# Kernel optimization log

Measured on AMD Instinct MI355X. Metric: run time of the kernel, lower is better.

The kernel has to match this reference:

```python
import jax, jax.numpy as jnp
import numpy as np

B, H, W, C, HEADS, WS, SS = 32, 56, 56, 512, 16, 7, 3
HID = 4 * C
N = WS * WS          # tokens per window = 49
NW = (H // WS) * (W // WS)  # windows per image = 64
HD = C // HEADS
SCALE = HD ** -0.5

def _rel_index():
    coords = np.stack(np.meshgrid(np.arange(WS), np.arange(WS), indexing='ij'))
    cf = coords.reshape(2, -1)
    rel = (cf[:, :, None] - cf[:, None, :]).transpose(1, 2, 0)
    rel[..., 0] += WS - 1
    rel[..., 1] += WS - 1
    rel[..., 0] *= 2 * WS - 1
    return rel.sum(-1)  # [N, N]

REL_IDX = _rel_index()

def _attn_mask():
    # standard Swin SW-MSA mask: label 3x3 shifted regions, diff labels -> -100
    img = np.zeros((H, W), dtype=np.float32)
    cnt = 0
    for hs in (slice(0, -WS), slice(-WS, -SS), slice(-SS, None)):
        for ws_ in (slice(0, -WS), slice(-WS, -SS), slice(-SS, None)):
            img[hs, ws_] = cnt
            cnt += 1
    mw = img.reshape(H // WS, WS, W // WS, WS).transpose(0, 2, 1, 3).reshape(NW, N)
    diff = mw[:, None, :] - mw[:, :, None]
    return jnp.asarray(np.where(diff != 0, -100.0, 0.0).astype(np.float32))  # [NW, N, N]

ATTN_MASK = _attn_mask()

def layernorm(x, g, b, eps=1e-5):
    m = jnp.mean(x, -1, keepdims=True)
    v = jnp.mean((x - m) ** 2, -1, keepdims=True)
    return (x - m) * jax.lax.rsqrt(v + eps) * g + b

def setup_inputs():
    key = jax.random.key(0)
    ks = jax.random.split(key, 8)
    f32 = jnp.float32
    return {
        'x': jax.random.normal(ks[0], (B, H * W, C), f32),
        'norm1_g': jnp.ones((C,), f32), 'norm1_b': jnp.zeros((C,), f32),
        'qkv_w': jax.random.normal(ks[1], (3 * C, C), f32) * 0.02,
        'qkv_b': jnp.zeros((3 * C,), f32),
        'rel_bias': jax.random.normal(ks[2], ((2 * WS - 1) ** 2, HEADS), f32) * 0.02,
        'proj_w': jax.random.normal(ks[3], (C, C), f32) * 0.02,
        'proj_b': jnp.zeros((C,), f32),
        'norm2_g': jnp.ones((C,), f32), 'norm2_b': jnp.zeros((C,), f32),
        'mlp_w1': jax.random.normal(ks[4], (HID, C), f32) * 0.02,
        'mlp_b1': jnp.zeros((HID,), f32),
        'mlp_w2': jax.random.normal(ks[5], (C, HID), f32) * 0.02,
        'mlp_b2': jnp.zeros((C,), f32),
    }

def reference(x, norm1_g, norm1_b, qkv_w, qkv_b, rel_bias, proj_w, proj_b,
              norm2_g, norm2_b, mlp_w1, mlp_b1, mlp_w2, mlp_b2):
    skip = x
    h = layernorm(x, norm1_g, norm1_b).reshape(B, H, W, C)
    h = jnp.roll(h, (-SS, -SS), axis=(1, 2))  # cyclic shift
    # window partition -> [B*NW, N, C]
    h = h.reshape(B, H // WS, WS, W // WS, WS, C).transpose(0, 1, 3, 2, 4, 5).reshape(B * NW, N, C)
    qkv = (h @ qkv_w.T + qkv_b).reshape(B * NW, N, 3, HEADS, HD).transpose(2, 0, 3, 1, 4)
    q, k, v = qkv[0] * SCALE, qkv[1], qkv[2]  # [B*NW, HEADS, N, HD]
    attn = jnp.einsum('whnd,whmd->whnm', q, k)
    bias = rel_bias[REL_IDX.reshape(-1)].reshape(N, N, HEADS).transpose(2, 0, 1)
    attn = attn + bias[None]
    attn = attn.reshape(B, NW, HEADS, N, N) + ATTN_MASK[None, :, None]
    attn = jax.nn.softmax(attn, axis=-1).reshape(B * NW, HEADS, N, N)
    h = jnp.einsum('whnm,whmd->whnd', attn, v).transpose(0, 2, 1, 3).reshape(B * NW, N, C)
    h = h @ proj_w.T + proj_b
    # window reverse + reverse cyclic shift
    h = h.reshape(B, H // WS, W // WS, WS, WS, C).transpose(0, 1, 3, 2, 4, 5).reshape(B, H, W, C)
    h = jnp.roll(h, (SS, SS), axis=(1, 2)).reshape(B, H * W, C)
    x = skip + h
    m = layernorm(x, norm2_g, norm2_b)
    m = jax.nn.gelu(m @ mlp_w1.T + mlp_b1, approximate=False) @ mlp_w2.T + mlp_b2
    return x + m
```

## Files before the change

### kernel.cpp

```cpp
#include <hip/hip_runtime.h>
#include <cstdint>
#include <cstddef>

#define DI __device__ __forceinline__

typedef __bf16 bf16_t;
typedef __bf16 bf16x8 __attribute__((ext_vector_type(8)));
typedef float f32x4 __attribute__((ext_vector_type(4)));

static constexpr float SCALE = 0.17677669529663687f;

DI bf16_t f2b(float f) {
  uint32_t u = __builtin_bit_cast(uint32_t, f);
  u += 0x7fffu + ((u >> 16) & 1u);
  return __builtin_bit_cast(bf16_t, (uint16_t)(u >> 16));
}

DI void gld16(const void* g, void* l) {
  __builtin_amdgcn_global_load_lds(
      (const __attribute__((address_space(1))) uint32_t*)g,
      (__attribute__((address_space(3))) uint32_t*)l, 16, 0, 0);
}

__global__ __launch_bounds__(256)
void cvtw(const float* __restrict__ in, bf16_t* __restrict__ out, int n) {
  int i = (blockIdx.x * 256 + threadIdx.x) * 4;
  if (i >= n) return;
  float4 v = *(const float4*)(in + i);
  ushort4 o;
  o.x = __builtin_bit_cast(uint16_t, f2b(v.x));
  o.y = __builtin_bit_cast(uint16_t, f2b(v.y));
  o.z = __builtin_bit_cast(uint16_t, f2b(v.z));
  o.w = __builtin_bit_cast(uint16_t, f2b(v.w));
  *(ushort4*)(out + i) = o;
}

__global__ __launch_bounds__(256)
void bias_pre(const float* __restrict__ rel, float* __restrict__ bf) {
  int idx = blockIdx.x * 256 + threadIdx.x;
  int head = idx >> 12, t1 = (idx >> 6) & 63, t2 = idx & 63;
  float v = -1e30f;
  if (t1 < 49 && t2 < 49) {
    int i1 = t1 / 7, j1 = t1 - i1 * 7, i2 = t2 / 7, j2 = t2 - i2 * 7;
    v = rel[((i1 - i2 + 6) * 13 + (j1 - j2 + 6)) * 16 + head];
  }
  bf[idx] = v;
}

template<bool WIN>
__global__ __launch_bounds__(128)
void ln_kernel(const float* __restrict__ in, const float* __restrict__ g,
               const float* __restrict__ be, bf16_t* __restrict__ out)
{
  const int r = blockIdx.x;
  const int tid = threadIdx.x;
  long srow;
  if (WIN) {
    int bw = r / 49, t = r - bw * 49;
    int b = bw >> 6, w = bw & 63;
    int wh = w >> 3, ww = w & 7;
    int i = t / 7, j = t - i * 7;
    int hs = wh * 7 + i + 3; if (hs >= 56) hs -= 56;
    int wsr = ww * 7 + j + 3; if (wsr >= 56) wsr -= 56;
    srow = (long)b * 3136 + hs * 56 + wsr;
  } else {
    srow = r;
  }
  const float4 v = *(const float4*)(in + srow * 512 + tid * 4);
  float s = v.x + v.y + v.z + v.w;
  float sq = v.x * v.x + v.y * v.y + v.z * v.z + v.w * v.w;
#pragma unroll
  for (int m = 1; m < 64; m <<= 1) { s += __shfl_xor(s, m); sq += __shfl_xor(sq, m); }
  __shared__ float ls[2], lq[2];
  if ((tid & 63) == 0) { ls[tid >> 6] = s; lq[tid >> 6] = sq; }
  __syncthreads();
  s = ls[0] + ls[1]; sq = lq[0] + lq[1];
  const float mean = s * (1.f / 512.f);
  const float rs = rsqrtf(sq * (1.f / 512.f) - mean * mean + 1e-5f);
  const float4 gg = *(const float4*)(g + tid * 4);
  const float4 bb = *(const float4*)(be + tid * 4);
  ushort4 o;
  o.x = __builtin_bit_cast(uint16_t, f2b((v.x - mean) * rs * gg.x + bb.x));
  o.y = __builtin_bit_cast(uint16_t, f2b((v.y - mean) * rs * gg.y + bb.y));
  o.z = __builtin_bit_cast(uint16_t, f2b((v.z - mean) * rs * gg.z + bb.z));
  o.w = __builtin_bit_cast(uint16_t, f2b((v.w - mean) * rs * gg.w + bb.w));
  *(ushort4*)(out + (long)r * 512 + tid * 4) = o;
}

#define MFMA16(a, b, c) __builtin_amdgcn_mfma_f32_16x16x32_bf16((a), (b), (c), 0, 0, 0)

template<int EPI>
__global__ __launch_bounds__(1024, 4)
void gemm256(const bf16_t* __restrict__ A, const bf16_t* __restrict__ Bw,
             const float* __restrict__ bias, const float* __restrict__ extra,
             void* __restrict__ out0, void* __restrict__ out1v, void* __restrict__ out2v,
             const int K, const int NBN)
{
  __shared__ __align__(128) bf16_t lds[8][8192];
  const int tid = threadIdx.x, lane = tid & 63, wave = tid >> 6;
  const int NT = K >> 5;

  const int xcd = blockIdx.x & 7, j = blockIdx.x >> 3;
  const int G = 32 / NBN;
  if (j >= G * NBN) return;
  const int bmo = j / NBN;
  const int bn = j - bmo * NBN;
  const int m0 = xcd * 49;
  const int tiles = (49 - bmo + G - 1) / G;
  const int ST = tiles * NT;

  const int srow = tid >> 2, slot = tid & 3;
  const int chunk = slot ^ ((srow >> 1) & 3);
  const size_t strideA = (size_t)G * 256 * K;

  const bf16_t* pAs = A + ((size_t)(m0 + bmo) * 256 + srow) * K + chunk * 8;
  const bf16_t* pBs = Bw + ((size_t)bn * 256 + srow) * K + chunk * 8;
  int sS = 0, ktS = 0;

#define STG() do { \
    if (sS < ST) { \
      gld16(pAs + ktS * 32, &lds[ktS & 3][tid * 8]); \
      gld16(pBs + ktS * 32, &lds[4 + (ktS & 3)][tid * 8]); \
      ++sS; if (++ktS == NT) { ktS = 0; pAs += strideA; } \
    } \
  } while (0)

  const int fr = lane & 15, fkc = lane >> 4;
  const int wr = wave >> 2, wc = wave & 3;
  const int slotq = (fkc ^ ((fr >> 1) & 3)) << 3;
  const int aoff = (wr * 64 + fr) * 32 + slotq;
  const int boff = (wc * 64 + fr) * 32 + slotq;

  f32x4 acc[4][4] = {};

  STG(); STG(); STG();
  asm volatile("s_waitcnt vmcnt(4)");
  __builtin_amdgcn_s_barrier();
  __builtin_amdgcn_sched_barrier(0);

  int sG = 0;
  int bmC = m0 + bmo;
  const int rq = fkc * 4;
  float bs[4];
#pragma unroll
  for (int n = 0; n < 4; ++n) bs[n] = bias[bn * 256 + wc * 64 + n * 16 + fr];

  for (int t = 0; t < tiles; ++t) {
#pragma unroll 4
    for (int kt = 0; kt < NT; ++kt) {
      bf16x8 af[4], bq[4];
#pragma unroll
      for (int m = 0; m < 4; ++m) af[m] = *(const bf16x8*)&lds[kt & 3][aoff + m * 512];
#pragma unroll
      for (int n = 0; n < 4; ++n) bq[n] = *(const bf16x8*)&lds[4 + (kt & 3)][boff + n * 512];
      STG();
      __builtin_amdgcn_sched_barrier(0);
      __builtin_amdgcn_s_barrier();
      asm volatile("s_waitcnt lgkmcnt(0)");
      __builtin_amdgcn_sched_barrier(0);
      __builtin_amdgcn_s_setprio(1);
#pragma unroll
      for (int m = 0; m < 4; ++m)
#pragma unroll
        for (int n = 0; n < 4; ++n)
          acc[m][n] = MFMA16(af[m], bq[n], acc[m][n]);
      __builtin_amdgcn_s_setprio(0);
      __builtin_amdgcn_sched_barrier(0);
      if (sG + 3 < ST)      asm volatile("s_waitcnt vmcnt(4)");
      else if (sG + 2 < ST) asm volatile("s_waitcnt vmcnt(2)");
      else                  asm volatile("s_waitcnt vmcnt(0)");
      __builtin_amdgcn_s_barrier();
      __builtin_amdgcn_sched_barrier(0);
      ++sG;
    }
#pragma unroll
    for (int m = 0; m < 4; ++m) {
#pragma unroll
      for (int jj4 = 0; jj4 < 4; ++jj4) {
        const int grow = bmC * 256 + wr * 64 + m * 16 + rq + jj4;
        long obase = 0;
        if (EPI == 0) {
          int bwi = grow / 49, t_ = grow - bwi * 49;
          obase = ((long)bwi * 784 + t_) * 32;
        } else if (EPI == 1) {
          int bwi = grow / 49, t_ = grow - bwi * 49;
          int b = bwi >> 6, w = bwi & 63;
          int wh = w >> 3, ww = w & 7;
          int i = t_ / 7, jj = t_ - i * 7;
          int hs = wh * 7 + i + 3; if (hs >= 56) hs -= 56;
          int wsr = ww * 7 + jj + 3; if (wsr >= 56) wsr -= 56;
          obase = ((long)b * 3136 + hs * 56 + wsr) * 512;
        } else if (EPI == 2) {
          obase = (long)grow * 2048;
        } else {
          obase = (long)grow * 512;
        }
#pragma unroll
        for (int n = 0; n < 4; ++n) {
          const int gcol = bn * 256 + wc * 64 + n * 16 + fr;
          float v = acc[m][n][jj4] + bs[n];
          if (EPI == 0) {
            int part = gcol >> 9, head = (gcol >> 5) & 15, d = gcol & 31;
            if (part == 0) v *= SCALE;
            bf16_t* dst = (bf16_t*)(part == 0 ? out0 : (part == 1 ? out1v : out2v));
            dst[obase + (long)head * 1568 + d] = f2b(v);
          } else if (EPI == 1) {
            ((float*)out0)[obase + gcol] = v + extra[obase + gcol];
          } else if (EPI == 2) {
            float m2 = v * v;
            float z = v * fmaf(0.07135481627f, m2, 1.59576912161f);
            float e = __expf(z);
            float rr = __builtin_amdgcn_rcpf(e + 1.0f);
            ((bf16_t*)out0)[obase + gcol] = f2b(fmaf(-v, rr, v));
          } else {
            ((float*)out0)[obase + gcol] = v + extra[obase + gcol];
          }
        }
      }
    }
#pragma unroll
    for (int m = 0; m < 4; ++m)
#pragma unroll
      for (int n = 0; n < 4; ++n) acc[m][n] = (f32x4){0.f, 0.f, 0.f, 0.f};
    bmC += G;
  }
#undef STG
}

__global__ __launch_bounds__(256)
void attn_kernel(const bf16_t* __restrict__ qb, const bf16_t* __restrict__ kb,
                 const bf16_t* __restrict__ vb, const float* __restrict__ biasf,
                 bf16_t* __restrict__ aout)
{
  __shared__ bf16_t Q[64 * 32];
  __shared__ bf16_t Kl[64 * 32];
  __shared__ bf16_t Vt[32 * 64];
  __shared__ bf16_t Pl[4][16 * 64];
  const int bid = blockIdx.x;
  const int bw = bid >> 4, head = bid & 15;
  const int tid = threadIdx.x, lane = tid & 63, wave = tid >> 6;
  {
    uint4 z = {0u, 0u, 0u, 0u};
    *(uint4*)&Q[tid * 8] = z;
    *(uint4*)&Kl[tid * 8] = z;
    *(uint4*)&Vt[tid * 8] = z;
  }
  __syncthreads();
  const bf16_t* qsrc = qb + (long)bid * (49 * 32);
  const bf16_t* ksrc = kb + (long)bid * (49 * 32);
  const bf16_t* vsrc = vb + (long)bid * (49 * 32);
  if (tid < 196) {
    *(uint4*)&Q[tid * 8] = *(const uint4*)(qsrc + tid * 8);
    *(uint4*)&Kl[tid * 8] = *(const uint4*)(ksrc + tid * 8);
  }
  for (int e = tid; e < 1568; e += 256) {
    int t = e >> 5, d = e & 31;
    Vt[d * 64 + t] = vsrc[e];
  }
  __syncthreads();
  const int fr = lane & 15, fk = (lane >> 4) * 8, rq = (lane >> 4) * 4;
  bf16x8 aq = *(const bf16x8*)&Q[(wave * 16 + fr) * 32 + fk];
  f32x4 s[4];
#pragma unroll
  for (int n = 0; n < 4; ++n) {
    bf16x8 bk = *(const bf16x8*)&Kl[(n * 16 + fr) * 32 + fk];
    f32x4 z = {0.f, 0.f, 0.f, 0.f};
    s[n] = __builtin_amdgcn_mfma_f32_16x16x32_bf16(aq, bk, z, 0, 0, 0);
  }
  const int w = bw & 63;
  const bool wh7 = ((w >> 3) == 7), ww7 = ((w & 7) == 7);
  const float* bh = biasf + head * 4096;
#pragma unroll
  for (int j = 0; j < 4; ++j) {
    const int row = wave * 16 + rq + j;
    int i1 = row / 7, j1 = row - i1 * 7;
    bool b1h = wh7 && (i1 >= 4), b1w = ww7 && (j1 >= 4);
    float pv[4];
    float mx = -3.0e38f;
#pragma unroll
    for (int n = 0; n < 4; ++n) {
      const int col = n * 16 + fr;
      float v = s[n][j] + bh[row * 64 + col];
      if (wh7 || ww7) {
        int i2 = col / 7, j2 = col - i2 * 7;
        bool b2h = wh7 && (i2 >= 4), b2w = ww7 && (j2 >= 4);
        if ((b1h != b2h) || (b1w != b2w)) v -= 100.f;
      }
      pv[n] = v;
      mx = fmaxf(mx, v);
    }
#pragma unroll
    for (int msk = 1; msk < 16; msk <<= 1) mx = fmaxf(mx, __shfl_xor(mx, msk));
    float sm = 0.f;
#pragma unroll
    for (int n = 0; n < 4; ++n) { pv[n] = __expf(pv[n] - mx); sm += pv[n]; }
#pragma unroll
    for (int msk = 1; msk < 16; msk <<= 1) sm += __shfl_xor(sm, msk);
    const float inv = 1.f / sm;
#pragma unroll
    for (int n = 0; n < 4; ++n)
      Pl[wave][(rq + j) * 64 + n * 16 + fr] = f2b(pv[n] * inv);
  }
  __syncthreads();
  f32x4 o[2] = {};
#pragma unroll
  for (int kk = 0; kk < 2; ++kk) {
    bf16x8 pa = *(const bf16x8*)&Pl[wave][fr * 64 + kk * 32 + fk];
#pragma unroll
    for (int dt = 0; dt < 2; ++dt) {
      bf16x8 vv = *(const bf16x8*)&Vt[(dt * 16 + fr) * 64 + kk * 32 + fk];
      o[dt] = __builtin_amdgcn_mfma_f32_16x16x32_bf16(pa, vv, o[dt], 0, 0, 0);
    }
  }
#pragma unroll
  for (int j = 0; j < 4; ++j) {
    const int t1 = wave * 16 + rq + j;
    if (t1 < 49) {
      bf16_t* dst = aout + ((long)bw * 49 + t1) * 512 + head * 32;
      dst[fr] = f2b(o[0][j]);
      dst[16 + fr] = f2b(o[1][j]);
    }
  }
}

extern "C" void kernel_launch(void* const* d_in, const int* in_sizes, int n_in,
                              void* d_out, int out_size, void* d_ws, size_t ws_size,
                              hipStream_t stream)
{
  const float* x      = (const float*)d_in[0];
  const float* n1g    = (const float*)d_in[1];
  const float* n1b    = (const float*)d_in[2];
  const float* qkv_w  = (const float*)d_in[3];
  const float* qkv_b  = (const float*)d_in[4];
  const float* rel    = (const float*)d_in[5];
  const float* proj_w = (const float*)d_in[6];
  const float* proj_b = (const float*)d_in[7];
  const float* n2g    = (const float*)d_in[8];
  const float* n2b    = (const float*)d_in[9];
  const float* w1     = (const float*)d_in[10];
  const float* b1     = (const float*)d_in[11];
  const float* w2     = (const float*)d_in[12];
  const float* b2     = (const float*)d_in[13];

  char* ws = (char*)d_ws;
  bf16_t* Wqkv  = (bf16_t*)(ws + 0);
  bf16_t* Wproj = (bf16_t*)(ws + 1572864);
  bf16_t* Wm1   = (bf16_t*)(ws + 2097152);
  bf16_t* Wm2   = (bf16_t*)(ws + 4194304);
  float*  biasf = (float*)(ws + 6291456);
  const size_t ABYTES = (size_t)100352 * 512 * 2;
  const size_t P1 = 8388608;
  const size_t P2 = P1 + ABYTES + 1048576;
  bf16_t* xw      = (bf16_t*)(ws + P1);
  bf16_t* qbuf    = (bf16_t*)(ws + P2);
  bf16_t* kbuf    = (bf16_t*)(ws + P2 + ABYTES);
  bf16_t* vbuf    = (bf16_t*)(ws + P2 + 2 * ABYTES);
  bf16_t* attnout = xw;
  bf16_t* h2      = xw;
  bf16_t* hidden  = qbuf;

  cvtw<<<768, 256, 0, stream>>>(qkv_w, Wqkv, 1536 * 512);
  cvtw<<<256, 256, 0, stream>>>(proj_w, Wproj, 512 * 512);
  cvtw<<<1024, 256, 0, stream>>>(w1, Wm1, 2048 * 512);
  cvtw<<<1024, 256, 0, stream>>>(w2, Wm2, 512 * 2048);
  bias_pre<<<256, 256, 0, stream>>>(rel, biasf);

  ln_kernel<true><<<100352, 128, 0, stream>>>(x, n1g, n1b, xw);
  gemm256<0><<<256, 1024, 0, stream>>>(xw, Wqkv, qkv_b, nullptr,
                                       qbuf, kbuf, vbuf, 512, 6);
  attn_kernel<<<32768, 256, 0, stream>>>(qbuf, kbuf, vbuf, biasf, attnout);
  gemm256<1><<<256, 1024, 0, stream>>>(attnout, Wproj, proj_b, x,
                                       d_out, nullptr, nullptr, 512, 2);
  ln_kernel<false><<<100352, 128, 0, stream>>>((const float*)d_out, n2g, n2b, h2);
  gemm256<2><<<256, 1024, 0, stream>>>(h2, Wm1, b1, nullptr,
                                       hidden, nullptr, nullptr, 512, 8);
  gemm256<3><<<256, 1024, 0, stream>>>(hidden, Wm2, b2, (const float*)d_out,
                                       d_out, nullptr, nullptr, 2048, 2);
}
```

Baseline: 1.385 ms.

## Restructure GEMMs with resident B panel and register-staged A prefetch

Replaces the generic 256x256 gemm with two specialized kernels. The K=512 GEMMs (QKV, proj, MLP1) use 256x128 tiles, keep the whole B panel resident in LDS for the life of the block, and stream A through registers into a double-buffered LDS tile. The K=2048 MLP2 GEMM gets its own 512-thread kernel with register-staged A and B double buffering. Replacing the async global-to-LDS loads with register staging is meant to reduce per-k-step B reloads and synchronization, at the cost of more registers, lower MFMA density per wave and a changed tile walk order.

```diff
diff --git a/kernel.cpp b/kernel.cpp
--- a/kernel.cpp
+++ b/kernel.cpp
@@ -14,12 +14,6 @@
   uint32_t u = __builtin_bit_cast(uint32_t, f);
   u += 0x7fffu + ((u >> 16) & 1u);
   return __builtin_bit_cast(bf16_t, (uint16_t)(u >> 16));
-}
-
-DI void gld16(const void* g, void* l) {
-  __builtin_amdgcn_global_load_lds(
-      (const __attribute__((address_space(1))) uint32_t*)g,
-      (__attribute__((address_space(3))) uint32_t*)l, 16, 0, 0);
 }
 
 __global__ __launch_bounds__(256)
@@ -90,141 +84,281 @@
 #define MFMA16(a, b, c) __builtin_amdgcn_mfma_f32_16x16x32_bf16((a), (b), (c), 0, 0, 0)
 
 template<int EPI>
+DI void epi_store(int grow, int gcol, float v, const float* extra,
+                  void* out0, void* out1v, void* out2v)
+{
+  long obase = 0;
+  if (EPI == 0) {
+    int bwi = grow / 49, t_ = grow - bwi * 49;
+    obase = ((long)bwi * 784 + t_) * 32;
+  } else if (EPI == 1) {
+    int bwi = grow / 49, t_ = grow - bwi * 49;
+    int b = bwi >> 6, w = bwi & 63;
+    int wh = w >> 3, ww = w & 7;
+    int i = t_ / 7, jj = t_ - i * 7;
+    int hs = wh * 7 + i + 3; if (hs >= 56) hs -= 56;
+    int wsr = ww * 7 + jj + 3; if (wsr >= 56) wsr -= 56;
+    obase = ((long)b * 3136 + hs * 56 + wsr) * 512;
+  } else if (EPI == 2) {
+    obase = (long)grow * 2048;
+  } else {
+    obase = (long)grow * 512;
+  }
+  if (EPI == 0) {
+    int part = gcol >> 9, head = (gcol >> 5) & 15, d = gcol & 31;
+    if (part == 0) v *= SCALE;
+    bf16_t* dst = (bf16_t*)(part == 0 ? out0 : (part == 1 ? out1v : out2v));
+    dst[obase + (long)head * 1568 + d] = f2b(v);
+  } else if (EPI == 1) {
+    ((float*)out0)[obase + gcol] = v + extra[obase + gcol];
+  } else if (EPI == 2) {
+    float m2 = v * v;
+    float z = v * fmaf(0.07135481627f, m2, 1.59576912161f);
+    float e = __expf(z);
+    float rr = __builtin_amdgcn_rcpf(e + 1.0f);
+    ((bf16_t*)out0)[obase + gcol] = f2b(fmaf(-v, rr, v));
+  } else {
+    ((float*)out0)[obase + gcol] = v + extra[obase + gcol];
+  }
+}
+
+template<int EPI, int NBN>
 __global__ __launch_bounds__(1024, 4)
-void gemm256(const bf16_t* __restrict__ A, const bf16_t* __restrict__ Bw,
-             const float* __restrict__ bias, const float* __restrict__ extra,
-             void* __restrict__ out0, void* __restrict__ out1v, void* __restrict__ out2v,
-             const int K, const int NBN)
+void gemmR(const bf16_t* __restrict__ A, const bf16_t* __restrict__ Bw,
+           const float* __restrict__ bias, const float* __restrict__ extra,
+           void* __restrict__ out0, void* __restrict__ out1v, void* __restrict__ out2v)
 {
-  __shared__ __align__(128) bf16_t lds[8][8192];
+  constexpr int K = 512;
+  __shared__ __align__(128) bf16_t Alds[2][8192];
+  __shared__ __align__(128) bf16_t Blds[16][4096];
   const int tid = threadIdx.x, lane = tid & 63, wave = tid >> 6;
-  const int NT = K >> 5;
-
-  const int xcd = blockIdx.x & 7, j = blockIdx.x >> 3;
-  const int G = 32 / NBN;
-  if (j >= G * NBN) return;
-  const int bmo = j / NBN;
-  const int bn = j - bmo * NBN;
-  const int m0 = xcd * 49;
-  const int tiles = (49 - bmo + G - 1) / G;
-  const int ST = tiles * NT;
+  const int nWalk = 256 / NBN;
+  const int j = blockIdx.x;
+  if (j >= nWalk * NBN) return;
+  const int bn = j % NBN;
+  const int bm0 = j / NBN;
+  const int tiles = (392 - bm0 + nWalk - 1) / nWalk;
+
+  {
+    const int prow = tid >> 3, ps8 = tid & 7;
+    const bf16_t* bsrc = Bw + (size_t)(bn * 128 + prow) * K + ps8 * 4;
+    const int wslot = (((ps8 >> 1) ^ ((prow >> 1) & 3)) << 4) + (ps8 & 1) * 8;
+    uint2 tmp[16];
+#pragma unroll
+    for (int r = 0; r < 16; ++r) tmp[r] = *(const uint2*)(bsrc + r * 32);
+#pragma unroll
+    for (int r = 0; r < 16; ++r)
+      *(uint2*)((char*)&Blds[r][0] + prow * 64 + wslot) = tmp[r];
+  }
+  asm volatile("s_waitcnt vmcnt(0)");
 
   const int srow = tid >> 2, slot = tid & 3;
-  const int chunk = slot ^ ((srow >> 1) & 3);
-  const size_t strideA = (size_t)G * 256 * K;
-
-  const bf16_t* pAs = A + ((size_t)(m0 + bmo) * 256 + srow) * K + chunk * 8;
-  const bf16_t* pBs = Bw + ((size_t)bn * 256 + srow) * K + chunk * 8;
-  int sS = 0, ktS = 0;
-
-#define STG() do { \
-    if (sS < ST) { \
-      gld16(pAs + ktS * 32, &lds[ktS & 3][tid * 8]); \
-      gld16(pBs + ktS * 32, &lds[4 + (ktS & 3)][tid * 8]); \
-      ++sS; if (++ktS == NT) { ktS = 0; pAs += strideA; } \
-    } \
+  const int wby = srow * 64 + (((slot ^ ((srow >> 1) & 3))) << 4);
+  const bf16_t* pAs = A + (size_t)(bm0 * 256 + srow) * K + slot * 8;
+  int ktS = 0, bmS = bm0;
+  uint4 aq[8];
+
+#define ADV() do { \
+    if (++ktS == 16) { ktS = 0; bmS += nWalk; if (bmS < 392) pAs += (size_t)nWalk * 131072; } \
   } while (0)
+#define LOADQ(U) do { aq[U] = *(const uint4*)(pAs + ktS * 32); ADV(); } while (0)
 
   const int fr = lane & 15, fkc = lane >> 4;
-  const int wr = wave >> 2, wc = wave & 3;
+  const int wr = wave >> 1, wc = wave & 1;
+  const int slotq = (fkc ^ ((fr >> 1) & 3)) << 3;
+  const int aoff = (wr * 32 + fr) * 32 + slotq;
+  const int boff = (wc * 64 + fr) * 32 + slotq;
+
+  f32x4 acc[2][4] = {};
+
+  LOADQ(0); LOADQ(1); LOADQ(2); LOADQ(3); LOADQ(4); LOADQ(5); LOADQ(6); LOADQ(7);
+  asm volatile("s_waitcnt vmcnt(7)");
+  __builtin_amdgcn_sched_barrier(0);
+  *(uint4*)((char*)&Alds[0][0] + wby) = aq[0];
+  asm volatile("s_waitcnt lgkmcnt(0)");
+  __builtin_amdgcn_s_barrier();
+  __builtin_amdgcn_sched_barrier(0);
+
+  const int rq = fkc * 4;
+  float bs[4];
+#pragma unroll
+  for (int n = 0; n < 4; ++n) bs[n] = bias[bn * 128 + wc * 64 + n * 16 + fr];
+
+  for (int t = 0; t < tiles; ++t) {
+#pragma unroll
+    for (int kt = 0; kt < 16; ++kt) {
+      const int u = kt & 7;
+      bf16x8 af0 = *(const bf16x8*)&Alds[kt & 1][aoff];
+      bf16x8 af1 = *(const bf16x8*)&Alds[kt & 1][aoff + 512];
+      bf16x8 b0 = *(const bf16x8*)&Blds[kt][boff];
+      bf16x8 b1 = *(const bf16x8*)&Blds[kt][boff + 512];
+      bf16x8 b2 = *(const bf16x8*)&Blds[kt][boff + 1024];
+      bf16x8 b3 = *(const bf16x8*)&Blds[kt][boff + 1536];
+      LOADQ(u);
+      asm volatile("s_waitcnt lgkmcnt(0)");
+      __builtin_amdgcn_sched_barrier(0);
+      __builtin_amdgcn_s_setprio(1);
+      acc[0][0] = MFMA16(af0, b0, acc[0][0]);
+      acc[0][1] = MFMA16(af0, b1, acc[0][1]);
+      acc[0][2] = MFMA16(af0, b2, acc[0][2]);
+      acc[0][3] = MFMA16(af0, b3, acc[0][3]);
+      acc[1][0] = MFMA16(af1, b0, acc[1][0]);
+      acc[1][1] = MFMA16(af1, b1, acc[1][1]);
+      acc[1][2] = MFMA16(af1, b2, acc[1][2]);
+      acc[1][3] = MFMA16(af1, b3, acc[1][3]);
+      __builtin_amdgcn_s_setprio(0);
+      __builtin_amdgcn_sched_barrier(0);
+      asm volatile("s_waitcnt vmcnt(7)");
+      __builtin_amdgcn_sched_barrier(0);
+      *(uint4*)((char*)&Alds[(kt + 1) & 1][0] + wby) = aq[(u + 1) & 7];
+      asm volatile("s_waitcnt lgkmcnt(0)");
+      __builtin_amdgcn_s_barrier();
+      __builtin_amdgcn_sched_barrier(0);
+    }
+    const int bmC = bm0 + t * nWalk;
+#pragma unroll
+    for (int m = 0; m < 2; ++m)
+#pragma unroll
+      for (int jj = 0; jj < 4; ++jj) {
+        const int grow = bmC * 256 + wr * 32 + m * 16 + rq + jj;
+#pragma unroll
+        for (int n = 0; n < 4; ++n) {
+          const int gcol = bn * 128 + wc * 64 + n * 16 + fr;
+          epi_store<EPI>(grow, gcol, acc[m][n][jj] + bs[n], extra, out0, out1v, out2v);
+        }
+      }
+#pragma unroll
+    for (int m = 0; m < 2; ++m)
+#pragma unroll
+      for (int n = 0; n < 4; ++n) acc[m][n] = (f32x4){0.f, 0.f, 0.f, 0.f};
+  }
+#undef LOADQ
+#undef ADV
+}
+
+__global__ __launch_bounds__(512, 2)
+void gemmS(const bf16_t* __restrict__ A, const bf16_t* __restrict__ Bw,
+           const float* __restrict__ bias, const float* __restrict__ extra,
+           void* __restrict__ out0)
+{
+  constexpr int K = 2048, NBN = 4, nWalk = 64;
+  __shared__ __align__(128) bf16_t Alds[2][8192];
+  __shared__ __align__(128) bf16_t Blds2[2][4096];
+  const int tid = threadIdx.x, lane = tid & 63, wave = tid >> 6;
+  const int j = blockIdx.x;
+  const int bn = j % NBN;
+  const int bm0 = j / NBN;
+  const int tiles = (392 - bm0 + nWalk - 1) / nWalk;
+
+  const int srow2 = tid >> 1, s0 = (tid & 1) * 2;
+  const int brow = tid >> 2, bslot = tid & 3;
+  const bf16_t* pA0 = A + (size_t)(bm0 * 256 + srow2) * K + s0 * 8;
+  const bf16_t* pB0 = Bw + (size_t)(bn * 128 + brow) * K + bslot * 8;
+  const int wbyA0 = srow2 * 64 + ((s0 ^ ((srow2 >> 1) & 3)) << 4);
+  const int wbyA1 = srow2 * 64 + (((s0 + 1) ^ ((srow2 >> 1) & 3)) << 4);
+  const int wbyB = brow * 64 + ((bslot ^ ((brow >> 1) & 3)) << 4);
+  int ktS = 0, bmS = bm0;
+  uint4 aqA0[8], aqA1[8], aqB[8];
+
+#define ADVS() do { \
+    if (++ktS == 64) { ktS = 0; bmS += nWalk; if (bmS < 392) pA0 += (size_t)nWalk * 524288; } \
+  } while (0)
+#define LOADQS(U) do { \
+    aqA0[U] = *(const uint4*)(pA0 + ktS * 32); \
+    aqA1[U] = *(const uint4*)(pA0 + ktS * 32 + 8); \
+    aqB[U]  = *(const uint4*)(pB0 + ktS * 32); \
+    ADVS(); \
+  } while (0)
+
+  const int fr = lane & 15, fkc = lane >> 4;
+  const int wr = wave >> 1, wc = wave & 1;
   const int slotq = (fkc ^ ((fr >> 1) & 3)) << 3;
   const int aoff = (wr * 64 + fr) * 32 + slotq;
   const int boff = (wc * 64 + fr) * 32 + slotq;
 
   f32x4 acc[4][4] = {};
 
-  STG(); STG(); STG();
-  asm volatile("s_waitcnt vmcnt(4)");
+  LOADQS(0); LOADQS(1); LOADQS(2); LOADQS(3);
+  LOADQS(4); LOADQS(5); LOADQS(6); LOADQS(7);
+  asm volatile("s_waitcnt vmcnt(21)");
+  __builtin_amdgcn_sched_barrier(0);
+  *(uint4*)((char*)&Alds[0][0] + wbyA0) = aqA0[0];
+  *(uint4*)((char*)&Alds[0][0] + wbyA1) = aqA1[0];
+  *(uint4*)((char*)&Blds2[0][0] + wbyB) = aqB[0];
+  asm volatile("s_waitcnt lgkmcnt(0)");
   __builtin_amdgcn_s_barrier();
   __builtin_amdgcn_sched_barrier(0);
 
-  int sG = 0;
-  int bmC = m0 + bmo;
   const int rq = fkc * 4;
   float bs[4];
 #pragma unroll
-  for (int n = 0; n < 4; ++n) bs[n] = bias[bn * 256 + wc * 64 + n * 16 + fr];
+  for (int n = 0; n < 4; ++n) bs[n] = bias[bn * 128 + wc * 64 + n * 16 + fr];
 
   for (int t = 0; t < tiles; ++t) {
-#pragma unroll 4
-    for (int kt = 0; kt < NT; ++kt) {
-      bf16x8 af[4], bq[4];
-#pragma unroll
-      for (int m = 0; m < 4; ++m) af[m] = *(const bf16x8*)&lds[kt & 3][aoff + m * 512];
-#pragma unroll
-      for (int n = 0; n < 4; ++n) bq[n] = *(const bf16x8*)&lds[4 + (kt & 3)][boff + n * 512];
-      STG();
-      __builtin_amdgcn_sched_barrier(0);
-      __builtin_amdgcn_s_barrier();
-      asm volatile("s_waitcnt lgkmcnt(0)");
-      __builtin_amdgcn_sched_barrier(0);
-      __builtin_amdgcn_s_setprio(1);
-#pragma unroll
-      for (int m = 0; m < 4; ++m)
-#pragma unroll
-        for (int n = 0; n < 4; ++n)
-          acc[m][n] = MFMA16(af[m], bq[n], acc[m][n]);
-      __builtin_amdgcn_s_setprio(0);
-      __builtin_amdgcn_sched_barrier(0);
-      if (sG + 3 < ST)      asm volatile("s_waitcnt vmcnt(4)");
-      else if (sG + 2 < ST) asm volatile("s_waitcnt vmcnt(2)");
-      else                  asm volatile("s_waitcnt vmcnt(0)");
-      __builtin_amdgcn_s_barrier();
-      __builtin_amdgcn_sched_barrier(0);
-      ++sG;
+#pragma unroll 1
+    for (int g = 0; g < 8; ++g) {
+#pragma unroll
+      for (int u = 0; u < 8; ++u) {
+        const int par = u & 1;
+        bf16x8 af0 = *(const bf16x8*)&Alds[par][aoff];
+        bf16x8 af1 = *(const bf16x8*)&Alds[par][aoff + 512];
+        bf16x8 af2 = *(const bf16x8*)&Alds[par][aoff + 1024];
+        bf16x8 af3 = *(const bf16x8*)&Alds[par][aoff + 1536];
+        bf16x8 b0 = *(const bf16x8*)&Blds2[par][boff];
+        bf16x8 b1 = *(const bf16x8*)&Blds2[par][boff + 512];
+        bf16x8 b2 = *(const bf16x8*)&Blds2[par][boff + 1024];
+        bf16x8 b3 = *(const bf16x8*)&Blds2[par][boff + 1536];
+        LOADQS(u);
+        asm volatile("s_waitcnt lgkmcnt(0)");
+        __builtin_amdgcn_sched_barrier(0);
+        __builtin_amdgcn_s_setprio(1);
+        acc[0][0] = MFMA16(af0, b0, acc[0][0]);
+        acc[0][1] = MFMA16(af0, b1, acc[0][1]);
+        acc[0][2] = MFMA16(af0, b2, acc[0][2]);
+        acc[0][3] = MFMA16(af0, b3, acc[0][3]);
+        acc[1][0] = MFMA16(af1, b0, acc[1][0]);
+        acc[1][1] = MFMA16(af1, b1, acc[1][1]);
+        acc[1][2] = MFMA16(af1, b2, acc[1][2]);
+        acc[1][3] = MFMA16(af1, b3, acc[1][3]);
+        acc[2][0] = MFMA16(af2, b0, acc[2][0]);
+        acc[2][1] = MFMA16(af2, b1, acc[2][1]);
+        acc[2][2] = MFMA16(af2, b2, acc[2][2]);
+        acc[2][3] = MFMA16(af2, b3, acc[2][3]);
+        acc[3][0] = MFMA16(af3, b0, acc[3][0]);
+        acc[3][1] = MFMA16(af3, b1, acc[3][1]);
+        acc[3][2] = MFMA16(af3, b2, acc[3][2]);
+        acc[3][3] = MFMA16(af3, b3, acc[3][3]);
+        __builtin_amdgcn_s_setprio(0);
+        __builtin_amdgcn_sched_barrier(0);
+        asm volatile("s_waitcnt vmcnt(21)");
+        __builtin_amdgcn_sched_barrier(0);
+        *(uint4*)((char*)&Alds[par ^ 1][0] + wbyA0) = aqA0[(u + 1) & 7];
+        *(uint4*)((char*)&Alds[par ^ 1][0] + wbyA1) = aqA1[(u + 1) & 7];
+        *(uint4*)((char*)&Blds2[par ^ 1][0] + wbyB) = aqB[(u + 1) & 7];
+        asm volatile("s_waitcnt lgkmcnt(0)");
+        __builtin_amdgcn_s_barrier();
+        __builtin_amdgcn_sched_barrier(0);
+      }
     }
-#pragma unroll
-    for (int m = 0; m < 4; ++m) {
-#pragma unroll
-      for (int jj4 = 0; jj4 < 4; ++jj4) {
-        const int grow = bmC * 256 + wr * 64 + m * 16 + rq + jj4;
-        long obase = 0;
-        if (EPI == 0) {
-          int bwi = grow / 49, t_ = grow - bwi * 49;
-          obase = ((long)bwi * 784 + t_) * 32;
-        } else if (EPI == 1) {
-          int bwi = grow / 49, t_ = grow - bwi * 49;
-          int b = bwi >> 6, w = bwi & 63;
-          int wh = w >> 3, ww = w & 7;
-          int i = t_ / 7, jj = t_ - i * 7;
-          int hs = wh * 7 + i + 3; if (hs >= 56) hs -= 56;
-          int wsr = ww * 7 + jj + 3; if (wsr >= 56) wsr -= 56;
-          obase = ((long)b * 3136 + hs * 56 + wsr) * 512;
-        } else if (EPI == 2) {
-          obase = (long)grow * 2048;
-        } else {
-          obase = (long)grow * 512;
-        }
+    const int bmC = bm0 + t * nWalk;
+#pragma unroll
+    for (int m = 0; m < 4; ++m)
+#pragma unroll
+      for (int jj = 0; jj < 4; ++jj) {
+        const int grow = bmC * 256 + wr * 64 + m * 16 + rq + jj;
 #pragma unroll
         for (int n = 0; n < 4; ++n) {
-          const int gcol = bn * 256 + wc * 64 + n * 16 + fr;
-          float v = acc[m][n][jj4] + bs[n];
-          if (EPI == 0) {
-            int part = gcol >> 9, head = (gcol >> 5) & 15, d = gcol & 31;
-            if (part == 0) v *= SCALE;
-            bf16_t* dst = (bf16_t*)(part == 0 ? out0 : (part == 1 ? out1v : out2v));
-            dst[obase + (long)head * 1568 + d] = f2b(v);
-          } else if (EPI == 1) {
-            ((float*)out0)[obase + gcol] = v + extra[obase + gcol];
-          } else if (EPI == 2) {
-            float m2 = v * v;
-            float z = v * fmaf(0.07135481627f, m2, 1.59576912161f);
-            float e = __expf(z);
-            float rr = __builtin_amdgcn_rcpf(e + 1.0f);
-            ((bf16_t*)out0)[obase + gcol] = f2b(fmaf(-v, rr, v));
-          } else {
-            ((float*)out0)[obase + gcol] = v + extra[obase + gcol];
-          }
+          const int gcol = bn * 128 + wc * 64 + n * 16 + fr;
+          epi_store<3>(grow, gcol, acc[m][n][jj] + bs[n], extra, out0, nullptr, nullptr);
         }
       }
-    }
 #pragma unroll
     for (int m = 0; m < 4; ++m)
 #pragma unroll
       for (int n = 0; n < 4; ++n) acc[m][n] = (f32x4){0.f, 0.f, 0.f, 0.f};
-    bmC += G;
-  }
-#undef STG
+  }
+#undef LOADQS
+#undef ADVS
 }
 
 __global__ __launch_bounds__(256)
@@ -366,14 +500,10 @@
   bias_pre<<<256, 256, 0, stream>>>(rel, biasf);
 
   ln_kernel<true><<<100352, 128, 0, stream>>>(x, n1g, n1b, xw);
-  gemm256<0><<<256, 1024, 0, stream>>>(xw, Wqkv, qkv_b, nullptr,
-                                       qbuf, kbuf, vbuf, 512, 6);
+  gemmR<0, 12><<<256, 1024, 0, stream>>>(xw, Wqkv, qkv_b, nullptr, qbuf, kbuf, vbuf);
   attn_kernel<<<32768, 256, 0, stream>>>(qbuf, kbuf, vbuf, biasf, attnout);
-  gemm256<1><<<256, 1024, 0, stream>>>(attnout, Wproj, proj_b, x,
-                                       d_out, nullptr, nullptr, 512, 2);
+  gemmR<1, 4><<<256, 1024, 0, stream>>>(attnout, Wproj, proj_b, x, d_out, nullptr, nullptr);
   ln_kernel<false><<<100352, 128, 0, stream>>>((const float*)d_out, n2g, n2b, h2);
-  gemm256<2><<<256, 1024, 0, stream>>>(h2, Wm1, b1, nullptr,
-                                       hidden, nullptr, nullptr, 512, 8);
-  gemm256<3><<<256, 1024, 0, stream>>>(hidden, Wm2, b2, (const float*)d_out,
-                                       d_out, nullptr, nullptr, 2048, 2);
-}
+  gemmR<2, 16><<<256, 1024, 0, stream>>>(h2, Wm1, b1, nullptr, hidden, nullptr, nullptr);
+  gemmS<<<256, 512, 0, stream>>>(hidden, Wm2, b2, (const float*)d_out, d_out);
+}
```

Measured after the change: 3.792 ms. 174% more time.

## Halve GEMM block to 8 waves with 128x64 per-wave tiles

Applied to the files above, without the earlier changes.

The 256x256 GEMM tile now runs on 512 threads (8 waves) instead of 1024. Each wave computes a 128x64 sub-tile with 8x4 MFMA accumulators, and each thread issues four LDS-direct global loads per stage instead of two. This raises operand reuse per wave and reduces per-block LDS read traffic and barrier participants. In exchange it doubles accumulator registers per thread, which limits occupancy, and gives fewer waves to hide latency. The epilogue is moved into a helper function with unchanged semantics.

```diff
diff --git a/kernel.cpp b/kernel.cpp
--- a/kernel.cpp
+++ b/kernel.cpp
@@ -90,13 +90,52 @@
 #define MFMA16(a, b, c) __builtin_amdgcn_mfma_f32_16x16x32_bf16((a), (b), (c), 0, 0, 0)
 
 template<int EPI>
-__global__ __launch_bounds__(1024, 4)
+DI void epi_store(int grow, int gcol, float v, const float* extra,
+                  void* out0, void* out1v, void* out2v)
+{
+  long obase = 0;
+  if (EPI == 0) {
+    int bwi = grow / 49, t_ = grow - bwi * 49;
+    obase = ((long)bwi * 784 + t_) * 32;
+  } else if (EPI == 1) {
+    int bwi = grow / 49, t_ = grow - bwi * 49;
+    int b = bwi >> 6, w = bwi & 63;
+    int wh = w >> 3, ww = w & 7;
+    int i = t_ / 7, jj = t_ - i * 7;
+    int hs = wh * 7 + i + 3; if (hs >= 56) hs -= 56;
+    int wsr = ww * 7 + jj + 3; if (wsr >= 56) wsr -= 56;
+    obase = ((long)b * 3136 + hs * 56 + wsr) * 512;
+  } else if (EPI == 2) {
+    obase = (long)grow * 2048;
+  } else {
+    obase = (long)grow * 512;
+  }
+  if (EPI == 0) {
+    int part = gcol >> 9, head = (gcol >> 5) & 15, d = gcol & 31;
+    if (part == 0) v *= SCALE;
+    bf16_t* dst = (bf16_t*)(part == 0 ? out0 : (part == 1 ? out1v : out2v));
+    dst[obase + (long)head * 1568 + d] = f2b(v);
+  } else if (EPI == 1) {
+    ((float*)out0)[obase + gcol] = v + extra[obase + gcol];
+  } else if (EPI == 2) {
+    float m2 = v * v;
+    float z = v * fmaf(0.07135481627f, m2, 1.59576912161f);
+    float e = __expf(z);
+    float rr = __builtin_amdgcn_rcpf(e + 1.0f);
+    ((bf16_t*)out0)[obase + gcol] = f2b(fmaf(-v, rr, v));
+  } else {
+    ((float*)out0)[obase + gcol] = v + extra[obase + gcol];
+  }
+}
+
+template<int EPI>
+__global__ __launch_bounds__(512, 2)
 void gemm256(const bf16_t* __restrict__ A, const bf16_t* __restrict__ Bw,
              const float* __restrict__ bias, const float* __restrict__ extra,
              void* __restrict__ out0, void* __restrict__ out1v, void* __restrict__ out2v,
              const int K, const int NBN)
 {
-  __shared__ __align__(128) bf16_t lds[8][8192];
+  __shared__ __align__(128) bf16_t lds[4][2][8192];
   const int tid = threadIdx.x, lane = tid & 63, wave = tid >> 6;
   const int NT = K >> 5;
 
@@ -111,6 +150,7 @@
 
   const int srow = tid >> 2, slot = tid & 3;
   const int chunk = slot ^ ((srow >> 1) & 3);
+  const size_t rowK = (size_t)128 * K;
   const size_t strideA = (size_t)G * 256 * K;
 
   const bf16_t* pAs = A + ((size_t)(m0 + bmo) * 256 + srow) * K + chunk * 8;
@@ -119,8 +159,13 @@
 
 #define STG() do { \
     if (sS < ST) { \
-      gld16(pAs + ktS * 32, &lds[ktS & 3][tid * 8]); \
-      gld16(pBs + ktS * 32, &lds[4 + (ktS & 3)][tid * 8]); \
+      const int _b = sS & 3; \
+      const bf16_t* _pa = pAs + ktS * 32; \
+      const bf16_t* _pb = pBs + ktS * 32; \
+      gld16(_pa, &lds[_b][0][tid * 8]); \
+      gld16(_pa + rowK, &lds[_b][0][tid * 8 + 4096]); \
+      gld16(_pb, &lds[_b][1][tid * 8]); \
+      gld16(_pb + rowK, &lds[_b][1][tid * 8 + 4096]); \
       ++sS; if (++ktS == NT) { ktS = 0; pAs += strideA; } \
     } \
   } while (0)
@@ -128,31 +173,32 @@
   const int fr = lane & 15, fkc = lane >> 4;
   const int wr = wave >> 2, wc = wave & 3;
   const int slotq = (fkc ^ ((fr >> 1) & 3)) << 3;
-  const int aoff = (wr * 64 + fr) * 32 + slotq;
+  const int aoff = (wr * 128 + fr) * 32 + slotq;
   const int boff = (wc * 64 + fr) * 32 + slotq;
 
-  f32x4 acc[4][4] = {};
+  f32x4 acc[8][4] = {};
 
   STG(); STG(); STG();
-  asm volatile("s_waitcnt vmcnt(4)");
+  asm volatile("s_waitcnt vmcnt(8)");
   __builtin_amdgcn_s_barrier();
   __builtin_amdgcn_sched_barrier(0);
 
   int sG = 0;
-  int bmC = m0 + bmo;
   const int rq = fkc * 4;
   float bs[4];
 #pragma unroll
   for (int n = 0; n < 4; ++n) bs[n] = bias[bn * 256 + wc * 64 + n * 16 + fr];
 
   for (int t = 0; t < tiles; ++t) {
+    const int bmC = m0 + bmo + t * G;
 #pragma unroll 4
     for (int kt = 0; kt < NT; ++kt) {
-      bf16x8 af[4], bq[4];
-#pragma unroll
-      for (int m = 0; m < 4; ++m) af[m] = *(const bf16x8*)&lds[kt & 3][aoff + m * 512];
-#pragma unroll
-      for (int n = 0; n < 4; ++n) bq[n] = *(const bf16x8*)&lds[4 + (kt & 3)][boff + n * 512];
+      const int b = kt & 3;
+      bf16x8 af[8], bq[4];
+#pragma unroll
+      for (int m = 0; m < 8; ++m) af[m] = *(const bf16x8*)&lds[b][0][aoff + m * 512];
+#pragma unroll
+      for (int n = 0; n < 4; ++n) bq[n] = *(const bf16x8*)&lds[b][1][boff + n * 512];
       STG();
       __builtin_amdgcn_sched_barrier(0);
       __builtin_amdgcn_s_barrier();
@@ -160,69 +206,34 @@
       __builtin_amdgcn_sched_barrier(0);
       __builtin_amdgcn_s_setprio(1);
 #pragma unroll
-      for (int m = 0; m < 4; ++m)
+      for (int m = 0; m < 8; ++m)
 #pragma unroll
         for (int n = 0; n < 4; ++n)
           acc[m][n] = MFMA16(af[m], bq[n], acc[m][n]);
       __builtin_amdgcn_s_setprio(0);
       __builtin_amdgcn_sched_barrier(0);
-      if (sG + 3 < ST)      asm volatile("s_waitcnt vmcnt(4)");
-      else if (sG + 2 < ST) asm volatile("s_waitcnt vmcnt(2)");
-      else                  asm volatile("s_waitcnt vmcnt(0)");
+      if (sG + 4 <= ST)      asm volatile("s_waitcnt vmcnt(8)");
+      else if (sG + 3 == ST) asm volatile("s_waitcnt vmcnt(4)");
+      else                   asm volatile("s_waitcnt vmcnt(0)");
       __builtin_amdgcn_s_barrier();
       __builtin_amdgcn_sched_barrier(0);
       ++sG;
     }
 #pragma unroll
-    for (int m = 0; m < 4; ++m) {
-#pragma unroll
-      for (int jj4 = 0; jj4 < 4; ++jj4) {
-        const int grow = bmC * 256 + wr * 64 + m * 16 + rq + jj4;
-        long obase = 0;
-        if (EPI == 0) {
-          int bwi = grow / 49, t_ = grow - bwi * 49;
-          obase = ((long)bwi * 784 + t_) * 32;
-        } else if (EPI == 1) {
-          int bwi = grow / 49, t_ = grow - bwi * 49;
-          int b = bwi >> 6, w = bwi & 63;
-          int wh = w >> 3, ww = w & 7;
-          int i = t_ / 7, jj = t_ - i * 7;
-          int hs = wh * 7 + i + 3; if (hs >= 56) hs -= 56;
-          int wsr = ww * 7 + jj + 3; if (wsr >= 56) wsr -= 56;
-          obase = ((long)b * 3136 + hs * 56 + wsr) * 512;
-        } else if (EPI == 2) {
-          obase = (long)grow * 2048;
-        } else {
-          obase = (long)grow * 512;
-        }
+    for (int m = 0; m < 8; ++m)
+#pragma unroll
+      for (int jj = 0; jj < 4; ++jj) {
+        const int grow = bmC * 256 + wr * 128 + m * 16 + rq + jj;
 #pragma unroll
         for (int n = 0; n < 4; ++n) {
           const int gcol = bn * 256 + wc * 64 + n * 16 + fr;
-          float v = acc[m][n][jj4] + bs[n];
-          if (EPI == 0) {
-            int part = gcol >> 9, head = (gcol >> 5) & 15, d = gcol & 31;
-            if (part == 0) v *= SCALE;
-            bf16_t* dst = (bf16_t*)(part == 0 ? out0 : (part == 1 ? out1v : out2v));
-            dst[obase + (long)head * 1568 + d] = f2b(v);
-          } else if (EPI == 1) {
-            ((float*)out0)[obase + gcol] = v + extra[obase + gcol];
-          } else if (EPI == 2) {
-            float m2 = v * v;
-            float z = v * fmaf(0.07135481627f, m2, 1.59576912161f);
-            float e = __expf(z);
-            float rr = __builtin_amdgcn_rcpf(e + 1.0f);
-            ((bf16_t*)out0)[obase + gcol] = f2b(fmaf(-v, rr, v));
-          } else {
-            ((float*)out0)[obase + gcol] = v + extra[obase + gcol];
-          }
+          epi_store<EPI>(grow, gcol, acc[m][n][jj] + bs[n], extra, out0, out1v, out2v);
         }
       }
-    }
-#pragma unroll
-    for (int m = 0; m < 4; ++m)
+#pragma unroll
+    for (int m = 0; m < 8; ++m)
 #pragma unroll
       for (int n = 0; n < 4; ++n) acc[m][n] = (f32x4){0.f, 0.f, 0.f, 0.f};
-    bmC += G;
   }
 #undef STG
 }
@@ -366,14 +377,14 @@
   bias_pre<<<256, 256, 0, stream>>>(rel, biasf);
 
   ln_kernel<true><<<100352, 128, 0, stream>>>(x, n1g, n1b, xw);
-  gemm256<0><<<256, 1024, 0, stream>>>(xw, Wqkv, qkv_b, nullptr,
-                                       qbuf, kbuf, vbuf, 512, 6);
+  gemm256<0><<<256, 512, 0, stream>>>(xw, Wqkv, qkv_b, nullptr,
+                                      qbuf, kbuf, vbuf, 512, 6);
   attn_kernel<<<32768, 256, 0, stream>>>(qbuf, kbuf, vbuf, biasf, attnout);
-  gemm256<1><<<256, 1024, 0, stream>>>(attnout, Wproj, proj_b, x,
-                                       d_out, nullptr, nullptr, 512, 2);
+  gemm256<1><<<256, 512, 0, stream>>>(attnout, Wproj, proj_b, x,
+                                      d_out, nullptr, nullptr, 512, 2);
   ln_kernel<false><<<100352, 128, 0, stream>>>((const float*)d_out, n2g, n2b, h2);
-  gemm256<2><<<256, 1024, 0, stream>>>(h2, Wm1, b1, nullptr,
-                                       hidden, nullptr, nullptr, 512, 8);
-  gemm256<3><<<256, 1024, 0, stream>>>(hidden, Wm2, b2, (const float*)d_out,
-                                       d_out, nullptr, nullptr, 2048, 2);
-}
+  gemm256<2><<<256, 512, 0, stream>>>(h2, Wm1, b1, nullptr,
+                                      hidden, nullptr, nullptr, 512, 8);
+  gemm256<3><<<256, 512, 0, stream>>>(hidden, Wm2, b2, (const float*)d_out,
+                                      d_out, nullptr, nullptr, 2048, 2);
+}
```

Result: no change. 1.377 ms (-0.6%).

## Replace direct-to-LDS GEMM with register-staged double-buffered 256x128 tiles

Applied to the files above, without the earlier changes.

The 256x256, 1024-thread GEMM that used global_load_lds with a 4-stage LDS ring is replaced by a 512-thread kernel using 256x128 tiles. Global loads now go into registers three k-steps ahead and are written into a two-slot LDS double buffer, with one barrier per k-step. Tiles are distributed across blocks as a flat (m,n) tile index strided by 32, and the epilogue moves into a helper function. The aim is better occupancy and balance, at the cost of more register pressure and extra LDS write instructions.

```diff
diff --git a/kernel.cpp b/kernel.cpp
--- a/kernel.cpp
+++ b/kernel.cpp
@@ -14,12 +14,6 @@
   uint32_t u = __builtin_bit_cast(uint32_t, f);
   u += 0x7fffu + ((u >> 16) & 1u);
   return __builtin_bit_cast(bf16_t, (uint16_t)(u >> 16));
-}
-
-DI void gld16(const void* g, void* l) {
-  __builtin_amdgcn_global_load_lds(
-      (const __attribute__((address_space(1))) uint32_t*)g,
-      (__attribute__((address_space(3))) uint32_t*)l, 16, 0, 0);
 }
 
 __global__ __launch_bounds__(256)
@@ -90,72 +84,121 @@
 #define MFMA16(a, b, c) __builtin_amdgcn_mfma_f32_16x16x32_bf16((a), (b), (c), 0, 0, 0)
 
 template<int EPI>
-__global__ __launch_bounds__(1024, 4)
-void gemm256(const bf16_t* __restrict__ A, const bf16_t* __restrict__ Bw,
-             const float* __restrict__ bias, const float* __restrict__ extra,
-             void* __restrict__ out0, void* __restrict__ out1v, void* __restrict__ out2v,
-             const int K, const int NBN)
-{
-  __shared__ __align__(128) bf16_t lds[8][8192];
+DI void epi_store(int grow, int gcol, float v, const float* extra,
+                  void* out0, void* out1v, void* out2v)
+{
+  long obase = 0;
+  if (EPI == 0) {
+    int bwi = grow / 49, t_ = grow - bwi * 49;
+    obase = ((long)bwi * 784 + t_) * 32;
+  } else if (EPI == 1) {
+    int bwi = grow / 49, t_ = grow - bwi * 49;
+    int b = bwi >> 6, w = bwi & 63;
+    int wh = w >> 3, ww = w & 7;
+    int i = t_ / 7, jj = t_ - i * 7;
+    int hs = wh * 7 + i + 3; if (hs >= 56) hs -= 56;
+    int wsr = ww * 7 + jj + 3; if (wsr >= 56) wsr -= 56;
+    obase = ((long)b * 3136 + hs * 56 + wsr) * 512;
+  } else if (EPI == 2) {
+    obase = (long)grow * 2048;
+  } else {
+    obase = (long)grow * 512;
+  }
+  if (EPI == 0) {
+    int part = gcol >> 9, head = (gcol >> 5) & 15, d = gcol & 31;
+    if (part == 0) v *= SCALE;
+    bf16_t* dst = (bf16_t*)(part == 0 ? out0 : (part == 1 ? out1v : out2v));
+    dst[obase + (long)head * 1568 + d] = f2b(v);
+  } else if (EPI == 1) {
+    ((float*)out0)[obase + gcol] = v + extra[obase + gcol];
+  } else if (EPI == 2) {
+    float m2 = v * v;
+    float z = v * fmaf(0.07135481627f, m2, 1.59576912161f);
+    float e = __expf(z);
+    float rr = __builtin_amdgcn_rcpf(e + 1.0f);
+    ((bf16_t*)out0)[obase + gcol] = f2b(fmaf(-v, rr, v));
+  } else {
+    ((float*)out0)[obase + gcol] = v + extra[obase + gcol];
+  }
+}
+
+template<int EPI, int NBN>
+__global__ __launch_bounds__(512, 2)
+void gemmP(const bf16_t* __restrict__ A, const bf16_t* __restrict__ Bw,
+           const float* __restrict__ bias, const float* __restrict__ extra,
+           void* __restrict__ out0, void* __restrict__ out1v, void* __restrict__ out2v,
+           const int K)
+{
+  __shared__ __align__(128) bf16_t ldsA[2][8192];
+  __shared__ __align__(128) bf16_t ldsB[2][4096];
   const int tid = threadIdx.x, lane = tid & 63, wave = tid >> 6;
   const int NT = K >> 5;
-
   const int xcd = blockIdx.x & 7, j = blockIdx.x >> 3;
-  const int G = 32 / NBN;
-  if (j >= G * NBN) return;
-  const int bmo = j / NBN;
-  const int bn = j - bmo * NBN;
   const int m0 = xcd * 49;
-  const int tiles = (49 - bmo + G - 1) / G;
-  const int ST = tiles * NT;
-
-  const int srow = tid >> 2, slot = tid & 3;
-  const int chunk = slot ^ ((srow >> 1) & 3);
-  const size_t strideA = (size_t)G * 256 * K;
-
-  const bf16_t* pAs = A + ((size_t)(m0 + bmo) * 256 + srow) * K + chunk * 8;
-  const bf16_t* pBs = Bw + ((size_t)bn * 256 + srow) * K + chunk * 8;
-  int sS = 0, ktS = 0;
-
-#define STG() do { \
-    if (sS < ST) { \
-      gld16(pAs + ktS * 32, &lds[ktS & 3][tid * 8]); \
-      gld16(pBs + ktS * 32, &lds[4 + (ktS & 3)][tid * 8]); \
-      ++sS; if (++ktS == NT) { ktS = 0; pAs += strideA; } \
+  const int ntileX = 49 * NBN;
+  const int tiles = (ntileX - j + 31) >> 5;
+
+  const int arow = tid >> 1, ac = (tid & 1) * 2;
+  const int brow = tid >> 2, bc = tid & 3;
+  const int awb0 = arow * 64 + ((ac ^ ((arow >> 1) & 3)) << 4);
+  const int awb1 = arow * 64 + (((ac + 1) ^ ((arow >> 1) & 3)) << 4);
+  const int bwb  = brow * 64 + ((bc ^ ((brow >> 1) & 3)) << 4);
+
+  int ktS = 0, tS = j;
+  const bf16_t* pA = A + ((size_t)(m0 + tS / NBN) * 256 + arow) * K + ac * 8;
+  const bf16_t* pB = Bw + ((size_t)(tS % NBN) * 128 + brow) * K + bc * 8;
+  uint4 qA0[4], qA1[4], qB[4];
+
+#define ISSUE(SLOT) do { \
+    qA0[SLOT] = *(const uint4*)(pA + ktS * 32); \
+    qA1[SLOT] = *(const uint4*)(pA + ktS * 32 + 8); \
+    qB[SLOT]  = *(const uint4*)(pB + ktS * 32); \
+    if (++ktS == NT) { \
+      ktS = 0; tS += 32; \
+      if (tS < ntileX) { \
+        pA = A + ((size_t)(m0 + tS / NBN) * 256 + arow) * K + ac * 8; \
+        pB = Bw + ((size_t)(tS % NBN) * 128 + brow) * K + bc * 8; \
+      } \
     } \
   } while (0)
 
+#define COMMIT(SLOT, BUF) do { \
+    *(uint4*)((char*)&ldsA[BUF][0] + awb0) = qA0[SLOT]; \
+    *(uint4*)((char*)&ldsA[BUF][0] + awb1) = qA1[SLOT]; \
+    *(uint4*)((char*)&ldsB[BUF][0] + bwb)  = qB[SLOT]; \
+  } while (0)
+
   const int fr = lane & 15, fkc = lane >> 4;
-  const int wr = wave >> 2, wc = wave & 3;
+  const int wr = wave >> 1, wc = wave & 1;
   const int slotq = (fkc ^ ((fr >> 1) & 3)) << 3;
   const int aoff = (wr * 64 + fr) * 32 + slotq;
   const int boff = (wc * 64 + fr) * 32 + slotq;
 
   f32x4 acc[4][4] = {};
 
-  STG(); STG(); STG();
-  asm volatile("s_waitcnt vmcnt(4)");
+  ISSUE(0); ISSUE(1); ISSUE(2);
+  COMMIT(0, 0);
+  asm volatile("s_waitcnt lgkmcnt(0)");
   __builtin_amdgcn_s_barrier();
   __builtin_amdgcn_sched_barrier(0);
 
-  int sG = 0;
-  int bmC = m0 + bmo;
   const int rq = fkc * 4;
-  float bs[4];
-#pragma unroll
-  for (int n = 0; n < 4; ++n) bs[n] = bias[bn * 256 + wc * 64 + n * 16 + fr];
 
   for (int t = 0; t < tiles; ++t) {
+    const int tauC = j + t * 32;
+    const int bmC = m0 + tauC / NBN;
+    const int bnC = tauC % NBN;
 #pragma unroll 4
     for (int kt = 0; kt < NT; ++kt) {
       bf16x8 af[4], bq[4];
 #pragma unroll
-      for (int m = 0; m < 4; ++m) af[m] = *(const bf16x8*)&lds[kt & 3][aoff + m * 512];
-#pragma unroll
-      for (int n = 0; n < 4; ++n) bq[n] = *(const bf16x8*)&lds[4 + (kt & 3)][boff + n * 512];
-      STG();
-      __builtin_amdgcn_sched_barrier(0);
-      __builtin_amdgcn_s_barrier();
+      for (int m = 0; m < 4; ++m) af[m] = *(const bf16x8*)&ldsA[kt & 1][aoff + m * 512];
+#pragma unroll
+      for (int n = 0; n < 4; ++n) bq[n] = *(const bf16x8*)&ldsB[kt & 1][boff + n * 512];
+      ISSUE((kt + 3) & 3);
+      __builtin_amdgcn_sched_barrier(0);
+      COMMIT((kt + 1) & 3, (kt + 1) & 1);
+      __builtin_amdgcn_sched_barrier(0);
       asm volatile("s_waitcnt lgkmcnt(0)");
       __builtin_amdgcn_sched_barrier(0);
       __builtin_amdgcn_s_setprio(1);
@@ -166,65 +209,30 @@
           acc[m][n] = MFMA16(af[m], bq[n], acc[m][n]);
       __builtin_amdgcn_s_setprio(0);
       __builtin_amdgcn_sched_barrier(0);
-      if (sG + 3 < ST)      asm volatile("s_waitcnt vmcnt(4)");
-      else if (sG + 2 < ST) asm volatile("s_waitcnt vmcnt(2)");
-      else                  asm volatile("s_waitcnt vmcnt(0)");
       __builtin_amdgcn_s_barrier();
       __builtin_amdgcn_sched_barrier(0);
-      ++sG;
     }
-#pragma unroll
-    for (int m = 0; m < 4; ++m) {
-#pragma unroll
-      for (int jj4 = 0; jj4 < 4; ++jj4) {
-        const int grow = bmC * 256 + wr * 64 + m * 16 + rq + jj4;
-        long obase = 0;
-        if (EPI == 0) {
-          int bwi = grow / 49, t_ = grow - bwi * 49;
-          obase = ((long)bwi * 784 + t_) * 32;
-        } else if (EPI == 1) {
-          int bwi = grow / 49, t_ = grow - bwi * 49;
-          int b = bwi >> 6, w = bwi & 63;
-          int wh = w >> 3, ww = w & 7;
-          int i = t_ / 7, jj = t_ - i * 7;
-          int hs = wh * 7 + i + 3; if (hs >= 56) hs -= 56;
-          int wsr = ww * 7 + jj + 3; if (wsr >= 56) wsr -= 56;
-          obase = ((long)b * 3136 + hs * 56 + wsr) * 512;
-        } else if (EPI == 2) {
-          obase = (long)grow * 2048;
-        } else {
-          obase = (long)grow * 512;
-        }
+    float bs[4];
+#pragma unroll
+    for (int n = 0; n < 4; ++n) bs[n] = bias[bnC * 128 + wc * 64 + n * 16 + fr];
+#pragma unroll
+    for (int m = 0; m < 4; ++m)
+#pragma unroll
+      for (int jj = 0; jj < 4; ++jj) {
+        const int grow = bmC * 256 + wr * 64 + m * 16 + rq + jj;
 #pragma unroll
         for (int n = 0; n < 4; ++n) {
-          const int gcol = bn * 256 + wc * 64 + n * 16 + fr;
-          float v = acc[m][n][jj4] + bs[n];
-          if (EPI == 0) {
-            int part = gcol >> 9, head = (gcol >> 5) & 15, d = gcol & 31;
-            if (part == 0) v *= SCALE;
-            bf16_t* dst = (bf16_t*)(part == 0 ? out0 : (part == 1 ? out1v : out2v));
-            dst[obase + (long)head * 1568 + d] = f2b(v);
-          } else if (EPI == 1) {
-            ((float*)out0)[obase + gcol] = v + extra[obase + gcol];
-          } else if (EPI == 2) {
-            float m2 = v * v;
-            float z = v * fmaf(0.07135481627f, m2, 1.59576912161f);
-            float e = __expf(z);
-            float rr = __builtin_amdgcn_rcpf(e + 1.0f);
-            ((bf16_t*)out0)[obase + gcol] = f2b(fmaf(-v, rr, v));
-          } else {
-            ((float*)out0)[obase + gcol] = v + extra[obase + gcol];
-          }
+          const int gcol = bnC * 128 + wc * 64 + n * 16 + fr;
+          epi_store<EPI>(grow, gcol, acc[m][n][jj] + bs[n], extra, out0, out1v, out2v);
         }
       }
-    }
 #pragma unroll
     for (int m = 0; m < 4; ++m)
 #pragma unroll
       for (int n = 0; n < 4; ++n) acc[m][n] = (f32x4){0.f, 0.f, 0.f, 0.f};
-    bmC += G;
-  }
-#undef STG
+  }
+#undef ISSUE
+#undef COMMIT
 }
 
 __global__ __launch_bounds__(256)
@@ -366,14 +374,14 @@
   bias_pre<<<256, 256, 0, stream>>>(rel, biasf);
 
   ln_kernel<true><<<100352, 128, 0, stream>>>(x, n1g, n1b, xw);
-  gemm256<0><<<256, 1024, 0, stream>>>(xw, Wqkv, qkv_b, nullptr,
-                                       qbuf, kbuf, vbuf, 512, 6);
+  gemmP<0, 12><<<256, 512, 0, stream>>>(xw, Wqkv, qkv_b, nullptr,
+                                        qbuf, kbuf, vbuf, 512);
   attn_kernel<<<32768, 256, 0, stream>>>(qbuf, kbuf, vbuf, biasf, attnout);
-  gemm256<1><<<256, 1024, 0, stream>>>(attnout, Wproj, proj_b, x,
-                                       d_out, nullptr, nullptr, 512, 2);
+  gemmP<1, 4><<<256, 512, 0, stream>>>(attnout, Wproj, proj_b, x,
+                                       d_out, nullptr, nullptr, 512);
   ln_kernel<false><<<100352, 128, 0, stream>>>((const float*)d_out, n2g, n2b, h2);
-  gemm256<2><<<256, 1024, 0, stream>>>(h2, Wm1, b1, nullptr,
-                                       hidden, nullptr, nullptr, 512, 8);
-  gemm256<3><<<256, 1024, 0, stream>>>(hidden, Wm2, b2, (const float*)d_out,
-                                       d_out, nullptr, nullptr, 2048, 2);
-}
+  gemmP<2, 16><<<256, 512, 0, stream>>>(h2, Wm1, b1, nullptr,
+                                        hidden, nullptr, nullptr, 512);
+  gemmP<3, 4><<<256, 512, 0, stream>>>(hidden, Wm2, b2, (const float*)d_out,
+                                       d_out, nullptr, nullptr, 2048);
+}
```

After: 4.301 ms. 3.1x slower.
